# Optimization experiments

Hardware: AMD Instinct MI355X
Metric: run time of the kernel (lower is better)

Reference implementation:

```python
import jax, jax.numpy as jnp
import numpy as np

B, C, H, W = 1024, 1024, 14, 14
A = 8          # adt_num (number of expert branches)
CH = C // 4    # expert bottleneck width


def setup_inputs() -> dict:
    key = jax.random.key(0)
    ks = jax.random.split(key, 5)
    s_in = 1.0 / np.sqrt(C)
    s_hid = 1.0 / np.sqrt(CH)
    return {
        "features": jax.random.normal(ks[0], (B, C, H, W), dtype=jnp.float32),
        "fc_w": jax.random.normal(ks[1], (A, C), dtype=jnp.float32) * s_in,
        "fc_b": jnp.zeros((A,), dtype=jnp.float32),
        "fc1_w": jax.random.normal(ks[2], (A, C, CH), dtype=jnp.float32) * s_in,
        "fc1_b": jnp.zeros((A, CH), dtype=jnp.float32),
        "fc2_w": jax.random.normal(ks[3], (A, CH, C), dtype=jnp.float32) * s_hid,
        "fc2_b": jnp.zeros((A, C), dtype=jnp.float32),
    }


def reference(features, fc_w, fc_b, fc1_w, fc1_b, fc2_w, fc2_b):
    # Global average pool over spatial dims: [B, C]
    pooled = jnp.mean(features.reshape(features.shape[0], features.shape[1], -1), axis=2)
    # All adt_num expert branches as one batched GEMM pair: [B, A, CH] -> [B, A, C]
    h = jax.nn.relu(jnp.einsum("bc,ach->bah", pooled, fc1_w) + fc1_b)
    expert = jnp.einsum("bah,ahc->bac", h, fc2_w) + fc2_b
    # Softmax gating over experts: [B, A]
    gate = jax.nn.softmax(pooled @ fc_w.T + fc_b, axis=1)
    # Gate-weighted sum of expert outputs: [B, C]
    mixed = jnp.einsum("ba,bac->bc", gate, expert)
    # Sigmoid channel gate + residual: out = x * sigmoid(mixed) + x
    scale = jax.nn.sigmoid(mixed)[:, :, None, None]
    return features * scale + features
```

## Files before the change

kernel.cpp:

```cpp
#include <hip/hip_runtime.h>

#define B_  1024
#define C_  1024
#define HW_ 196
#define A_  8
#define CH_ 256
#define N1_ 2048
#define K2_ 2048

typedef __attribute__((ext_vector_type(8))) short short8;
typedef __attribute__((ext_vector_type(4))) float f32x4;

static __device__ __forceinline__ unsigned short f2bf(float x) {
  union { float f; unsigned u; } v; v.f = x;
  unsigned r = (v.u + 0x7FFFu + ((v.u >> 16) & 1u)) >> 16;
  return (unsigned short)r;
}

__global__ __launch_bounds__(256) void pooltc_k(const float* __restrict__ f,
                                                float* __restrict__ pooled,
                                                unsigned short* __restrict__ pooledb,
                                                const float* __restrict__ fc1_w,
                                                const float* __restrict__ fc2_w,
                                                unsigned short* __restrict__ w1t,
                                                unsigned short* __restrict__ w2t) {
  __shared__ float tile[32][33];
  if (blockIdx.x < 4096) {
    unsigned row = blockIdx.x * 256 + threadIdx.x;
    const f32x4* p = (const f32x4*)f + (size_t)row * 49;
    float s = 0.f;
    #pragma unroll 3
    for (int j = 0; j < 12; ++j) {
      f32x4 a = p[4 * j + 0], b = p[4 * j + 1], c = p[4 * j + 2], d = p[4 * j + 3];
      s += (a.x + a.y) + (a.z + a.w);
      s += (b.x + b.y) + (b.z + b.w);
      s += (c.x + c.y) + (c.z + c.w);
      s += (d.x + d.y) + (d.z + d.w);
    }
    f32x4 e = p[48];
    s += (e.x + e.y) + (e.z + e.w);
    float m = s * (1.0f / 196.0f);
    pooled[row] = m;
    pooledb[row] = f2bf(m);
  } else {
    int t = blockIdx.x - 4096;
    const float* in; unsigned short* out; int Cc, OS, c0, r0;
    if (t < 2048) {
      int z = t >> 8, rem = t & 255;
      in  = fc1_w + (size_t)z * (C_ * CH_);
      out = w1t   + (size_t)z * (CH_ * C_);
      Cc = CH_; OS = C_;
      c0 = (rem & 7) * 32;  r0 = (rem >> 3) * 32;
    } else {
      t -= 2048;
      int z = t >> 8, rem = t & 255;
      in  = fc2_w + (size_t)z * (CH_ * C_);
      out = w2t   + (size_t)z * CH_;
      Cc = C_; OS = K2_;
      c0 = (rem & 31) * 32; r0 = (rem >> 5) * 32;
    }
    int tx = threadIdx.x & 31, ty = threadIdx.x >> 5;
    #pragma unroll
    for (int i = 0; i < 32; i += 8)
      tile[ty + i][tx] = in[(size_t)(r0 + ty + i) * Cc + c0 + tx];
    __syncthreads();
    #pragma unroll
    for (int i = 0; i < 32; i += 8)
      out[(size_t)(c0 + ty + i) * OS + r0 + tx] = f2bf(tile[tx][ty + i]);
  }
}

__global__ void gate_k(const float* __restrict__ pooled, const float* __restrict__ fc_w,
                       const float* __restrict__ fc_b, float* __restrict__ gate) {
  __shared__ float dots[A_];
  int b = blockIdx.x;
  int wave = threadIdx.x >> 6, lane = threadIdx.x & 63;
  const float* p = pooled + (size_t)b * C_;
  for (int e = wave; e < A_; e += 4) {
    const float* wrow = fc_w + (size_t)e * C_;
    float sum = 0.f;
    for (int c = lane; c < C_; c += 64) sum += p[c] * wrow[c];
    #pragma unroll
    for (int off = 32; off > 0; off >>= 1) sum += __shfl_down(sum, off, 64);
    if (lane == 0) dots[e] = sum + fc_b[e];
  }
  __syncthreads();
  if (threadIdx.x == 0) {
    float mx = dots[0];
    for (int e = 1; e < A_; ++e) mx = fmaxf(mx, dots[e]);
    float ex[A_], se = 0.f;
    for (int e = 0; e < A_; ++e) { ex[e] = __expf(dots[e] - mx); se += ex[e]; }
    float inv = 1.0f / se;
    for (int e = 0; e < A_; ++e) gate[(size_t)b * A_ + e] = ex[e] * inv;
  }
}

__global__ __launch_bounds__(256) void gemm1_k(const unsigned short* __restrict__ Ab,
                                               const unsigned short* __restrict__ Bt,
                                               const float* __restrict__ fc1_b,
                                               const float* __restrict__ gate,
                                               unsigned short* __restrict__ gh) {
  int w = threadIdx.x >> 6, lane = threadIdx.x & 63;
  int r = lane & 15, kg = lane >> 4;
  int brow = blockIdx.x * 64 + (w >> 1) * 32;
  int bcol = blockIdx.y * 64 + (w & 1) * 32;
  const short8* Ap0 = (const short8*)(Ab + (size_t)(brow + r) * C_ + kg * 8);
  const short8* Ap1 = (const short8*)(Ab + (size_t)(brow + 16 + r) * C_ + kg * 8);
  const short8* Bp0 = (const short8*)(Bt + (size_t)(bcol + r) * C_ + kg * 8);
  const short8* Bp1 = (const short8*)(Bt + (size_t)(bcol + 16 + r) * C_ + kg * 8);
  f32x4 acc[2][2];
  acc[0][0] = (f32x4){0,0,0,0}; acc[0][1] = acc[0][0];
  acc[1][0] = acc[0][0];        acc[1][1] = acc[0][0];
  #pragma unroll 4
  for (int k = 0; k < C_ / 32; ++k) {
    short8 a0 = Ap0[4 * k], a1 = Ap1[4 * k];
    short8 b0 = Bp0[4 * k], b1 = Bp1[4 * k];
    acc[0][0] = __builtin_amdgcn_mfma_f32_16x16x32_bf16(a0, b0, acc[0][0], 0, 0, 0);
    acc[0][1] = __builtin_amdgcn_mfma_f32_16x16x32_bf16(a0, b1, acc[0][1], 0, 0, 0);
    acc[1][0] = __builtin_amdgcn_mfma_f32_16x16x32_bf16(a1, b0, acc[1][0], 0, 0, 0);
    acc[1][1] = __builtin_amdgcn_mfma_f32_16x16x32_bf16(a1, b1, acc[1][1], 0, 0, 0);
  }
  #pragma unroll
  for (int mi = 0; mi < 2; ++mi)
    #pragma unroll
    for (int ni = 0; ni < 2; ++ni) {
      int col = bcol + ni * 16 + r;
      int aidx = col >> 8;
      float bias = fc1_b[col];
      #pragma unroll
      for (int reg = 0; reg < 4; ++reg) {
        int row = brow + mi * 16 + kg * 4 + reg;
        float val = acc[mi][ni][reg] + bias;
        val = fmaxf(val, 0.f) * gate[row * A_ + aidx];
        gh[(size_t)row * N1_ + col] = f2bf(val);
      }
    }
}

__global__ __launch_bounds__(256) void gemm2_k(const unsigned short* __restrict__ Ab,
                                               const unsigned short* __restrict__ Bt,
                                               const float* __restrict__ gate,
                                               const float* __restrict__ fc2_b,
                                               float* __restrict__ s_out) {
  int w = threadIdx.x >> 6, lane = threadIdx.x & 63;
  int r = lane & 15, kg = lane >> 4;
  int brow = blockIdx.x * 64 + (w >> 1) * 32;
  int bcol = blockIdx.y * 64 + (w & 1) * 32;
  const short8* Ap0 = (const short8*)(Ab + (size_t)(brow + r) * K2_ + kg * 8);
  const short8* Ap1 = (const short8*)(Ab + (size_t)(brow + 16 + r) * K2_ + kg * 8);
  const short8* Bp0 = (const short8*)(Bt + (size_t)(bcol + r) * K2_ + kg * 8);
  const short8* Bp1 = (const short8*)(Bt + (size_t)(bcol + 16 + r) * K2_ + kg * 8);
  f32x4 acc[2][2];
  acc[0][0] = (f32x4){0,0,0,0}; acc[0][1] = acc[0][0];
  acc[1][0] = acc[0][0];        acc[1][1] = acc[0][0];
  #pragma unroll 4
  for (int k = 0; k < K2_ / 32; ++k) {
    short8 a0 = Ap0[4 * k], a1 = Ap1[4 * k];
    short8 b0 = Bp0[4 * k], b1 = Bp1[4 * k];
    acc[0][0] = __builtin_amdgcn_mfma_f32_16x16x32_bf16(a0, b0, acc[0][0], 0, 0, 0);
    acc[0][1] = __builtin_amdgcn_mfma_f32_16x16x32_bf16(a0, b1, acc[0][1], 0, 0, 0);
    acc[1][0] = __builtin_amdgcn_mfma_f32_16x16x32_bf16(a1, b0, acc[1][0], 0, 0, 0);
    acc[1][1] = __builtin_amdgcn_mfma_f32_16x16x32_bf16(a1, b1, acc[1][1], 0, 0, 0);
  }
  #pragma unroll
  for (int mi = 0; mi < 2; ++mi)
    #pragma unroll
    for (int ni = 0; ni < 2; ++ni) {
      int col = bcol + ni * 16 + r;
      float b8[A_];
      #pragma unroll
      for (int a = 0; a < A_; ++a) b8[a] = fc2_b[a * C_ + col];
      #pragma unroll
      for (int reg = 0; reg < 4; ++reg) {
        int row = brow + mi * 16 + kg * 4 + reg;
        const float* g = gate + (size_t)row * A_;
        float bias = 0.f;
        #pragma unroll
        for (int a = 0; a < A_; ++a) bias += g[a] * b8[a];
        float mixed = acc[mi][ni][reg] + bias;
        s_out[(size_t)row * C_ + col] = 1.0f + 1.0f / (1.0f + __expf(-mixed));
      }
    }
}

__global__ __launch_bounds__(256) void apply_k(const f32x4* __restrict__ f,
                                               const float* __restrict__ s,
                                               f32x4* __restrict__ out, unsigned total4) {
  unsigned i = blockIdx.x * 256 + threadIdx.x;
  unsigned stride = gridDim.x * 256;
  for (; i < total4; i += stride) {
    f32x4 v = __builtin_nontemporal_load(&f[i]);
    float m = s[i / 49u];
    v *= m;
    __builtin_nontemporal_store(v, &out[i]);
  }
}

extern "C" void kernel_launch(void* const* d_in, const int* in_sizes, int n_in,
                              void* d_out, int out_size, void* d_ws, size_t ws_size,
                              hipStream_t stream) {
  const float* features = (const float*)d_in[0];
  const float* fc_w  = (const float*)d_in[1];
  const float* fc_b  = (const float*)d_in[2];
  const float* fc1_w = (const float*)d_in[3];
  const float* fc1_b = (const float*)d_in[4];
  const float* fc2_w = (const float*)d_in[5];
  const float* fc2_b = (const float*)d_in[6];
  float* out = (float*)d_out;
  char* ws = (char*)d_ws;

  float*          pooled  = (float*)(ws);
  unsigned short* pooledb = (unsigned short*)(ws + 0x400000);
  float*          gate    = (float*)(ws + 0x600000);
  unsigned short* gh      = (unsigned short*)(ws + 0x610000);
  unsigned short* w1t     = (unsigned short*)(ws + 0xA10000);
  unsigned short* w2t     = (unsigned short*)(ws + 0xE10000);
  float*          s_buf   = (float*)(ws + 0x1210000);

  pooltc_k<<<8192, 256, 0, stream>>>(features, pooled, pooledb, fc1_w, fc2_w, w1t, w2t);
  gate_k<<<B_, 256, 0, stream>>>(pooled, fc_w, fc_b, gate);
  gemm1_k<<<dim3(16, 32), 256, 0, stream>>>(pooledb, w1t, fc1_b, gate, gh);
  gemm2_k<<<dim3(16, 16), 256, 0, stream>>>(gh, w2t, gate, fc2_b, s_buf);
  apply_k<<<8192, 256, 0, stream>>>((const f32x4*)features, s_buf, (f32x4*)out,
                                    (unsigned)(out_size / 4));
}
```

Baseline: 554.5 us.

## Pre-tile GEMM operands into MFMA fragment layout for contiguous per-wave loads

GEMM operands (pooled activations, both weight transposes, and the intermediate gh) are now written in a tiled layout where each 16x32 MFMA fragment occupies 512 contiguous bf16 values. Each wave's per-k load then becomes one fully coalesced 1 KB read instead of strided row reads. The bf16 conversion of pooled moves into extra blocks of the gate kernel. The cost is more complex index math in producers, scattered 2-byte stores in gemm1's epilogue, and half-idle threads in the transpose blocks.

```diff
diff --git a/kernel.cpp b/kernel.cpp
--- a/kernel.cpp
+++ b/kernel.cpp
@@ -11,6 +11,9 @@
 typedef __attribute__((ext_vector_type(8))) short short8;
 typedef __attribute__((ext_vector_type(4))) float f32x4;
 
+#define KT1 32
+#define KT2 64
+
 static __device__ __forceinline__ unsigned short f2bf(float x) {
   union { float f; unsigned u; } v; v.f = x;
   unsigned r = (v.u + 0x7FFFu + ((v.u >> 16) & 1u)) >> 16;
@@ -19,7 +22,6 @@
 
 __global__ __launch_bounds__(256) void pooltc_k(const float* __restrict__ f,
                                                 float* __restrict__ pooled,
-                                                unsigned short* __restrict__ pooledb,
                                                 const float* __restrict__ fc1_w,
                                                 const float* __restrict__ fc2_w,
                                                 unsigned short* __restrict__ w1t,
@@ -39,140 +41,165 @@
     }
     f32x4 e = p[48];
     s += (e.x + e.y) + (e.z + e.w);
-    float m = s * (1.0f / 196.0f);
-    pooled[row] = m;
-    pooledb[row] = f2bf(m);
+    pooled[row] = s * (1.0f / 196.0f);
   } else {
     int t = blockIdx.x - 4096;
-    const float* in; unsigned short* out; int Cc, OS, c0, r0;
+    const float* in; unsigned short* outb; int Cc, nt0, kt, KT;
     if (t < 2048) {
-      int z = t >> 8, rem = t & 255;
-      in  = fc1_w + (size_t)z * (C_ * CH_);
-      out = w1t   + (size_t)z * (CH_ * C_);
-      Cc = CH_; OS = C_;
-      c0 = (rem & 7) * 32;  r0 = (rem >> 3) * 32;
+      int a = t >> 8, rem = t & 255;
+      int c0 = (rem & 7) * 32, k0 = (rem >> 3) * 32;
+      in  = fc1_w + (size_t)a * (C_ * CH_) + (size_t)k0 * CH_ + c0;
+      Cc = CH_;
+      nt0 = a * 16 + (c0 >> 4);  kt = k0 >> 5;  KT = KT1;  outb = w1t;
     } else {
       t -= 2048;
-      int z = t >> 8, rem = t & 255;
-      in  = fc2_w + (size_t)z * (CH_ * C_);
-      out = w2t   + (size_t)z * CH_;
-      Cc = C_; OS = K2_;
-      c0 = (rem & 31) * 32; r0 = (rem >> 5) * 32;
+      int a = t >> 8, rem = t & 255;
+      int c0 = (rem & 31) * 32, ch0 = (rem >> 5) * 32;
+      in  = fc2_w + (size_t)a * (CH_ * C_) + (size_t)ch0 * C_ + c0;
+      Cc = C_;
+      nt0 = c0 >> 4;  kt = a * 8 + (ch0 >> 5);  KT = KT2;  outb = w2t;
     }
     int tx = threadIdx.x & 31, ty = threadIdx.x >> 5;
     #pragma unroll
     for (int i = 0; i < 32; i += 8)
-      tile[ty + i][tx] = in[(size_t)(r0 + ty + i) * Cc + c0 + tx];
+      tile[ty + i][tx] = in[(size_t)(ty + i) * Cc + tx];
     __syncthreads();
-    #pragma unroll
-    for (int i = 0; i < 32; i += 8)
-      out[(size_t)(c0 + ty + i) * OS + r0 + tx] = f2bf(tile[tx][ty + i]);
+    int tt = threadIdx.x;
+    if (tt < 128) {
+      int ct = tt >> 6, kg = (tt >> 4) & 3, r = tt & 15;
+      short8 v;
+      #pragma unroll
+      for (int j = 0; j < 8; ++j)
+        v[j] = (short)f2bf(tile[kg * 8 + j][ct * 16 + r]);
+      size_t base = ((size_t)(nt0 + ct) * KT + kt) * 512 + (size_t)(kg * 16 + r) * 8;
+      *(short8*)(outb + base) = v;
+    }
   }
 }
 
 __global__ void gate_k(const float* __restrict__ pooled, const float* __restrict__ fc_w,
-                       const float* __restrict__ fc_b, float* __restrict__ gate) {
+                       const float* __restrict__ fc_b, float* __restrict__ gate,
+                       unsigned short* __restrict__ a1t) {
   __shared__ float dots[A_];
-  int b = blockIdx.x;
-  int wave = threadIdx.x >> 6, lane = threadIdx.x & 63;
-  const float* p = pooled + (size_t)b * C_;
-  for (int e = wave; e < A_; e += 4) {
-    const float* wrow = fc_w + (size_t)e * C_;
-    float sum = 0.f;
-    for (int c = lane; c < C_; c += 64) sum += p[c] * wrow[c];
-    #pragma unroll
-    for (int off = 32; off > 0; off >>= 1) sum += __shfl_down(sum, off, 64);
-    if (lane == 0) dots[e] = sum + fc_b[e];
-  }
-  __syncthreads();
-  if (threadIdx.x == 0) {
-    float mx = dots[0];
-    for (int e = 1; e < A_; ++e) mx = fmaxf(mx, dots[e]);
-    float ex[A_], se = 0.f;
-    for (int e = 0; e < A_; ++e) { ex[e] = __expf(dots[e] - mx); se += ex[e]; }
-    float inv = 1.0f / se;
-    for (int e = 0; e < A_; ++e) gate[(size_t)b * A_ + e] = ex[e] * inv;
-  }
-}
-
-__global__ __launch_bounds__(256) void gemm1_k(const unsigned short* __restrict__ Ab,
-                                               const unsigned short* __restrict__ Bt,
+  if (blockIdx.x < 1024) {
+    int b = blockIdx.x;
+    int wave = threadIdx.x >> 6, lane = threadIdx.x & 63;
+    const float* p = pooled + (size_t)b * C_;
+    for (int e = wave; e < A_; e += 4) {
+      const float* wrow = fc_w + (size_t)e * C_;
+      float sum = 0.f;
+      for (int c = lane; c < C_; c += 64) sum += p[c] * wrow[c];
+      #pragma unroll
+      for (int off = 32; off > 0; off >>= 1) sum += __shfl_down(sum, off, 64);
+      if (lane == 0) dots[e] = sum + fc_b[e];
+    }
+    __syncthreads();
+    if (threadIdx.x == 0) {
+      float mx = dots[0];
+      for (int e = 1; e < A_; ++e) mx = fmaxf(mx, dots[e]);
+      float ex[A_], se = 0.f;
+      for (int e = 0; e < A_; ++e) { ex[e] = __expf(dots[e] - mx); se += ex[e]; }
+      float inv = 1.0f / se;
+      for (int e = 0; e < A_; ++e) gate[(size_t)b * A_ + e] = ex[e] * inv;
+    }
+  } else {
+    int h = blockIdx.x - 1024;
+    int rt = h >> 1, kt0 = (h & 1) * 16;
+    int t = threadIdx.x;
+    int e0 = 2 * t;
+    int kg = e0 >> 7, r = (e0 >> 3) & 15, j0 = e0 & 7;
+    int row = rt * 16 + r;
+    for (int kt = kt0; kt < kt0 + 16; ++kt) {
+      int col = kt * 32 + kg * 8 + j0;
+      float v0 = pooled[(size_t)row * C_ + col];
+      float v1 = pooled[(size_t)row * C_ + col + 1];
+      size_t base = ((size_t)rt * KT1 + kt) * 512 + e0;
+      a1t[base]     = f2bf(v0);
+      a1t[base + 1] = f2bf(v1);
+    }
+  }
+}
+
+__global__ __launch_bounds__(256) void gemm1_k(const unsigned short* __restrict__ A1,
+                                               const unsigned short* __restrict__ W1,
                                                const float* __restrict__ fc1_b,
                                                const float* __restrict__ gate,
                                                unsigned short* __restrict__ gh) {
   int w = threadIdx.x >> 6, lane = threadIdx.x & 63;
-  int r = lane & 15, kg = lane >> 4;
-  int brow = blockIdx.x * 64 + (w >> 1) * 32;
-  int bcol = blockIdx.y * 64 + (w & 1) * 32;
-  const short8* Ap0 = (const short8*)(Ab + (size_t)(brow + r) * C_ + kg * 8);
-  const short8* Ap1 = (const short8*)(Ab + (size_t)(brow + 16 + r) * C_ + kg * 8);
-  const short8* Bp0 = (const short8*)(Bt + (size_t)(bcol + r) * C_ + kg * 8);
-  const short8* Bp1 = (const short8*)(Bt + (size_t)(bcol + 16 + r) * C_ + kg * 8);
+  int rt0 = blockIdx.x * 4 + (w >> 1) * 2;
+  int nt0 = blockIdx.y * 4 + (w & 1) * 2;
+  const short8* Ap0 = (const short8*)(A1 + (size_t)(rt0    ) * KT1 * 512 + lane * 8);
+  const short8* Ap1 = (const short8*)(A1 + (size_t)(rt0 + 1) * KT1 * 512 + lane * 8);
+  const short8* Bp0 = (const short8*)(W1 + (size_t)(nt0    ) * KT1 * 512 + lane * 8);
+  const short8* Bp1 = (const short8*)(W1 + (size_t)(nt0 + 1) * KT1 * 512 + lane * 8);
   f32x4 acc[2][2];
   acc[0][0] = (f32x4){0,0,0,0}; acc[0][1] = acc[0][0];
   acc[1][0] = acc[0][0];        acc[1][1] = acc[0][0];
   #pragma unroll 4
-  for (int k = 0; k < C_ / 32; ++k) {
-    short8 a0 = Ap0[4 * k], a1 = Ap1[4 * k];
-    short8 b0 = Bp0[4 * k], b1 = Bp1[4 * k];
+  for (int kt = 0; kt < KT1; ++kt) {
+    short8 a0 = Ap0[64 * kt], a1 = Ap1[64 * kt];
+    short8 b0 = Bp0[64 * kt], b1 = Bp1[64 * kt];
     acc[0][0] = __builtin_amdgcn_mfma_f32_16x16x32_bf16(a0, b0, acc[0][0], 0, 0, 0);
     acc[0][1] = __builtin_amdgcn_mfma_f32_16x16x32_bf16(a0, b1, acc[0][1], 0, 0, 0);
     acc[1][0] = __builtin_amdgcn_mfma_f32_16x16x32_bf16(a1, b0, acc[1][0], 0, 0, 0);
     acc[1][1] = __builtin_amdgcn_mfma_f32_16x16x32_bf16(a1, b1, acc[1][1], 0, 0, 0);
   }
+  int r = lane & 15, kg = lane >> 4;
   #pragma unroll
   for (int mi = 0; mi < 2; ++mi)
     #pragma unroll
     for (int ni = 0; ni < 2; ++ni) {
-      int col = bcol + ni * 16 + r;
+      int col = (nt0 + ni) * 16 + r;
+      float bias = fc1_b[col];
       int aidx = col >> 8;
-      float bias = fc1_b[col];
       #pragma unroll
       for (int reg = 0; reg < 4; ++reg) {
-        int row = brow + mi * 16 + kg * 4 + reg;
+        int row = (rt0 + mi) * 16 + kg * 4 + reg;
         float val = acc[mi][ni][reg] + bias;
         val = fmaxf(val, 0.f) * gate[row * A_ + aidx];
-        gh[(size_t)row * N1_ + col] = f2bf(val);
+        size_t idx = ((size_t)(row >> 4) * KT2 + (col >> 5)) * 512
+                   + (size_t)((col >> 3) & 3) * 128 + (size_t)(row & 15) * 8 + (col & 7);
+        gh[idx] = f2bf(val);
       }
     }
 }
 
-__global__ __launch_bounds__(256) void gemm2_k(const unsigned short* __restrict__ Ab,
-                                               const unsigned short* __restrict__ Bt,
+__global__ __launch_bounds__(256) void gemm2_k(const unsigned short* __restrict__ GH,
+                                               const unsigned short* __restrict__ W2,
                                                const float* __restrict__ gate,
                                                const float* __restrict__ fc2_b,
                                                float* __restrict__ s_out) {
   int w = threadIdx.x >> 6, lane = threadIdx.x & 63;
-  int r = lane & 15, kg = lane >> 4;
-  int brow = blockIdx.x * 64 + (w >> 1) * 32;
-  int bcol = blockIdx.y * 64 + (w & 1) * 32;
-  const short8* Ap0 = (const short8*)(Ab + (size_t)(brow + r) * K2_ + kg * 8);
-  const short8* Ap1 = (const short8*)(Ab + (size_t)(brow + 16 + r) * K2_ + kg * 8);
-  const short8* Bp0 = (const short8*)(Bt + (size_t)(bcol + r) * K2_ + kg * 8);
-  const short8* Bp1 = (const short8*)(Bt + (size_t)(bcol + 16 + r) * K2_ + kg * 8);
+  int rt0 = blockIdx.x * 4 + (w >> 1) * 2;
+  int nt0 = blockIdx.y * 4 + (w & 1) * 2;
+  const short8* Ap0 = (const short8*)(GH + (size_t)(rt0    ) * KT2 * 512 + lane * 8);
+  const short8* Ap1 = (const short8*)(GH + (size_t)(rt0 + 1) * KT2 * 512 + lane * 8);
+  const short8* Bp0 = (const short8*)(W2 + (size_t)(nt0    ) * KT2 * 512 + lane * 8);
+  const short8* Bp1 = (const short8*)(W2 + (size_t)(nt0 + 1) * KT2 * 512 + lane * 8);
   f32x4 acc[2][2];
   acc[0][0] = (f32x4){0,0,0,0}; acc[0][1] = acc[0][0];
   acc[1][0] = acc[0][0];        acc[1][1] = acc[0][0];
   #pragma unroll 4
-  for (int k = 0; k < K2_ / 32; ++k) {
-    short8 a0 = Ap0[4 * k], a1 = Ap1[4 * k];
-    short8 b0 = Bp0[4 * k], b1 = Bp1[4 * k];
+  for (int kt = 0; kt < KT2; ++kt) {
+    short8 a0 = Ap0[64 * kt], a1 = Ap1[64 * kt];
+    short8 b0 = Bp0[64 * kt], b1 = Bp1[64 * kt];
     acc[0][0] = __builtin_amdgcn_mfma_f32_16x16x32_bf16(a0, b0, acc[0][0], 0, 0, 0);
     acc[0][1] = __builtin_amdgcn_mfma_f32_16x16x32_bf16(a0, b1, acc[0][1], 0, 0, 0);
     acc[1][0] = __builtin_amdgcn_mfma_f32_16x16x32_bf16(a1, b0, acc[1][0], 0, 0, 0);
     acc[1][1] = __builtin_amdgcn_mfma_f32_16x16x32_bf16(a1, b1, acc[1][1], 0, 0, 0);
   }
+  int r = lane & 15, kg = lane >> 4;
   #pragma unroll
   for (int mi = 0; mi < 2; ++mi)
     #pragma unroll
     for (int ni = 0; ni < 2; ++ni) {
-      int col = bcol + ni * 16 + r;
+      int col = (nt0 + ni) * 16 + r;
       float b8[A_];
       #pragma unroll
       for (int a = 0; a < A_; ++a) b8[a] = fc2_b[a * C_ + col];
       #pragma unroll
       for (int reg = 0; reg < 4; ++reg) {
-        int row = brow + mi * 16 + kg * 4 + reg;
+        int row = (rt0 + mi) * 16 + kg * 4 + reg;
         const float* g = gate + (size_t)row * A_;
         float bias = 0.f;
         #pragma unroll
@@ -209,17 +236,17 @@
   float* out = (float*)d_out;
   char* ws = (char*)d_ws;
 
-  float*          pooled  = (float*)(ws);
-  unsigned short* pooledb = (unsigned short*)(ws + 0x400000);
-  float*          gate    = (float*)(ws + 0x600000);
-  unsigned short* gh      = (unsigned short*)(ws + 0x610000);
-  unsigned short* w1t     = (unsigned short*)(ws + 0xA10000);
-  unsigned short* w2t     = (unsigned short*)(ws + 0xE10000);
-  float*          s_buf   = (float*)(ws + 0x1210000);
-
-  pooltc_k<<<8192, 256, 0, stream>>>(features, pooled, pooledb, fc1_w, fc2_w, w1t, w2t);
-  gate_k<<<B_, 256, 0, stream>>>(pooled, fc_w, fc_b, gate);
-  gemm1_k<<<dim3(16, 32), 256, 0, stream>>>(pooledb, w1t, fc1_b, gate, gh);
+  float*          pooled = (float*)(ws);
+  unsigned short* a1t    = (unsigned short*)(ws + 0x400000);
+  float*          gate   = (float*)(ws + 0x600000);
+  unsigned short* gh     = (unsigned short*)(ws + 0x610000);
+  unsigned short* w1t    = (unsigned short*)(ws + 0xA10000);
+  unsigned short* w2t    = (unsigned short*)(ws + 0xE10000);
+  float*          s_buf  = (float*)(ws + 0x1210000);
+
+  pooltc_k<<<8192, 256, 0, stream>>>(features, pooled, fc1_w, fc2_w, w1t, w2t);
+  gate_k<<<1152, 256, 0, stream>>>(pooled, fc_w, fc_b, gate, a1t);
+  gemm1_k<<<dim3(16, 32), 256, 0, stream>>>(a1t, w1t, fc1_b, gate, gh);
   gemm2_k<<<dim3(16, 16), 256, 0, stream>>>(gh, w2t, gate, fc2_b, s_buf);
   apply_k<<<8192, 256, 0, stream>>>((const f32x4*)features, s_buf, (f32x4*)out,
                                     (unsigned)(out_size / 4));
```

After: 515.0 us (median of 3 runs). 7.1% less time.
